# Kernel tuning notes

Measured on AMD Instinct MI355X. Metric: run time of the kernel, lower is better.

Reference implementation:

```python
import jax, jax.numpy as jnp
import numpy as np

EMBED_DIM = 1024
PROJ_DIM = 512
NUM_HEADS = 8
HEAD_DIM = PROJ_DIM // NUM_HEADS
B, L = 2, 2048


def setup_inputs() -> dict:
    key = jax.random.key(0)
    ks = jax.random.split(key, 7)
    s = lambda d: 1.0 / np.sqrt(d)
    return {
        "x": jax.random.normal(ks[0], (B, L, EMBED_DIM), jnp.float32),
        "proj_W": jax.random.normal(ks[1], (EMBED_DIM, PROJ_DIM), jnp.float32) * s(EMBED_DIM),
        "proj_b": jax.random.normal(ks[2], (PROJ_DIM,), jnp.float32) * 0.01,
        "attn_Wq": jax.random.normal(ks[3], (PROJ_DIM, NUM_HEADS, HEAD_DIM), jnp.float32) * s(PROJ_DIM),
        "attn_Wk": jax.random.normal(ks[4], (PROJ_DIM, NUM_HEADS, HEAD_DIM), jnp.float32) * s(PROJ_DIM),
        "attn_Wv": jax.random.normal(ks[5], (PROJ_DIM, NUM_HEADS, HEAD_DIM), jnp.float32) * s(PROJ_DIM),
        "out_W": jax.random.normal(ks[6], (NUM_HEADS * HEAD_DIM, EMBED_DIM), jnp.float32) * s(NUM_HEADS * HEAD_DIM),
    }


def reference(x, proj_W, proj_b, attn_Wq, attn_Wk, attn_Wv, out_W):
    # ReLU projection: (B, L, embed_dim) -> (B, L, proj_dim)
    p = jax.nn.relu(x @ proj_W + proj_b)
    # Per-head projections: (B, L, C) x (C, H, Dh) -> (B, H, L, Dh)
    q = jnp.einsum('blc,chd->bhld', p, attn_Wq)
    k = jnp.einsum('blc,chd->bhld', p, attn_Wk)
    v = jnp.einsum('blc,chd->bhld', p, attn_Wv)
    scale = 1.0 / np.sqrt(HEAD_DIM).astype(np.float32)
    scores = jnp.einsum('bhqd,bhkd->bhqk', q, k) * scale  # (B, H, L, L)
    weights = jax.nn.softmax(scores, axis=-1)
    heads = jnp.einsum('bhqk,bhkd->bhqd', weights, v)  # (B, H, L, Dh)
    heads = heads.transpose(0, 2, 1, 3).reshape(p.shape[0], p.shape[1], NUM_HEADS * HEAD_DIM)
    return heads @ out_W  # (B, L, embed_dim)
```

## Files before the change

### kernel.cpp

```cpp
#include <hip/hip_runtime.h>
#include <math.h>

#define BATCH 2
#define SEQ 2048
#define BL (BATCH * SEQ)
#define EMBED 1024
#define PROJ 512
#define NHEADS 8
#define HDIM 64
#define QKVN (3 * PROJ)

typedef _Float16 half8 __attribute__((ext_vector_type(8)));
typedef float floatx4 __attribute__((ext_vector_type(4)));

__global__ __launch_bounds__(256) void trconv(const float* __restrict__ src,
                                              _Float16* __restrict__ dst,
                                              int K, int N, float scale) {
    __shared__ float tile[64][65];
    const int t  = threadIdx.x;
    const int n0 = blockIdx.x * 64;
    const int k0 = blockIdx.y * 64;
    const int tx = t & 63;
    const int ty = t >> 6;
#pragma unroll
    for (int i = 0; i < 16; ++i) {
        int k = ty * 16 + i;
        tile[k][tx] = src[(size_t)(k0 + k) * N + n0 + tx];
    }
    __syncthreads();
#pragma unroll
    for (int i = 0; i < 16; ++i) {
        int n = ty * 16 + i;
        dst[(size_t)(n0 + n) * K + k0 + tx] = (_Float16)(tile[tx][n] * scale);
    }
}

__global__ __launch_bounds__(256) void trans_v(const _Float16* __restrict__ v,
                                               _Float16* __restrict__ vt) {
    __shared__ _Float16 tile[64][72];
    const int t  = threadIdx.x;
    const int t0 = blockIdx.x * 64;
    const int h  = blockIdx.y;
    const int b  = blockIdx.z;
    {
        const int r = t >> 2, c0 = (t & 3) * 16;
        const _Float16* src = v + (size_t)(b * SEQ + t0 + r) * QKVN + h * HDIM + c0;
        *reinterpret_cast<half8*>(&tile[r][c0])     = *reinterpret_cast<const half8*>(src);
        *reinterpret_cast<half8*>(&tile[r][c0 + 8]) = *reinterpret_cast<const half8*>(src + 8);
    }
    __syncthreads();
    {
        const int c = t >> 2, k0 = (t & 3) * 16;
        half8 o1, o2;
#pragma unroll
        for (int i = 0; i < 8; ++i) { o1[i] = tile[k0 + i][c]; o2[i] = tile[k0 + 8 + i][c]; }
        _Float16* dst = vt + ((size_t)(b * NHEADS + h) * HDIM + c) * SEQ + t0 + k0;
        *reinterpret_cast<half8*>(dst)     = o1;
        *reinterpret_cast<half8*>(dst + 8) = o2;
    }
}

template <int A_F32, int BIASRELU, int C_F32>
__global__ __launch_bounds__(256) void gemm_mfma(const void* __restrict__ Ap,
                                                 const _Float16* __restrict__ Bt,
                                                 const float* __restrict__ bias,
                                                 void* __restrict__ Cp,
                                                 int M, int N, int K) {
    __shared__ _Float16 Ah[64][40];
    __shared__ _Float16 Bh[128][40];

    const int t  = threadIdx.x;
    const int w  = t >> 6;
    const int l  = t & 63;
    const int lr = l & 15;
    const int lg = l >> 4;
    const int bm = blockIdx.y * 64;
    const int bn = blockIdx.x * 128;
    const int wr = w >> 1;
    const int wc = w & 1;

    const int ar = t >> 2, ac = (t & 3) * 8;
    const int br = t >> 1, bc = (t & 1) * 16;

    floatx4 acc[2][4];
#pragma unroll
    for (int i = 0; i < 2; ++i)
#pragma unroll
        for (int j = 0; j < 4; ++j) acc[i][j] = (floatx4){0.f, 0.f, 0.f, 0.f};

    float4 af0, af1;
    half8 areg, breg0, breg1;

    const float* Af = (const float*)Ap;
    const _Float16* Ah16 = (const _Float16*)Ap;

    if (A_F32) {
        af0 = *reinterpret_cast<const float4*>(&Af[(size_t)(bm + ar) * K + ac]);
        af1 = *reinterpret_cast<const float4*>(&Af[(size_t)(bm + ar) * K + ac + 4]);
    } else {
        areg = *reinterpret_cast<const half8*>(&Ah16[(size_t)(bm + ar) * K + ac]);
    }
    breg0 = *reinterpret_cast<const half8*>(&Bt[(size_t)(bn + br) * K + bc]);
    breg1 = *reinterpret_cast<const half8*>(&Bt[(size_t)(bn + br) * K + bc + 8]);

    for (int kt = 0; kt < K; kt += 32) {
        if (A_F32) {
            half8 hcv;
            hcv[0] = (_Float16)af0.x; hcv[1] = (_Float16)af0.y;
            hcv[2] = (_Float16)af0.z; hcv[3] = (_Float16)af0.w;
            hcv[4] = (_Float16)af1.x; hcv[5] = (_Float16)af1.y;
            hcv[6] = (_Float16)af1.z; hcv[7] = (_Float16)af1.w;
            *reinterpret_cast<half8*>(&Ah[ar][ac]) = hcv;
        } else {
            *reinterpret_cast<half8*>(&Ah[ar][ac]) = areg;
        }
        *reinterpret_cast<half8*>(&Bh[br][bc])     = breg0;
        *reinterpret_cast<half8*>(&Bh[br][bc + 8]) = breg1;
        __syncthreads();

        if (kt + 32 < K) {
            if (A_F32) {
                af0 = *reinterpret_cast<const float4*>(&Af[(size_t)(bm + ar) * K + kt + 32 + ac]);
                af1 = *reinterpret_cast<const float4*>(&Af[(size_t)(bm + ar) * K + kt + 32 + ac + 4]);
            } else {
                areg = *reinterpret_cast<const half8*>(&Ah16[(size_t)(bm + ar) * K + kt + 32 + ac]);
            }
            breg0 = *reinterpret_cast<const half8*>(&Bt[(size_t)(bn + br) * K + kt + 32 + bc]);
            breg1 = *reinterpret_cast<const half8*>(&Bt[(size_t)(bn + br) * K + kt + 32 + bc + 8]);
        }

        half8 afr[2], bfr[4];
#pragma unroll
        for (int mf = 0; mf < 2; ++mf)
            afr[mf] = *reinterpret_cast<const half8*>(&Ah[wr * 32 + mf * 16 + lr][lg * 8]);
#pragma unroll
        for (int nf = 0; nf < 4; ++nf)
            bfr[nf] = *reinterpret_cast<const half8*>(&Bh[wc * 64 + nf * 16 + lr][lg * 8]);
#pragma unroll
        for (int mf = 0; mf < 2; ++mf)
#pragma unroll
            for (int nf = 0; nf < 4; ++nf)
                acc[mf][nf] = __builtin_amdgcn_mfma_f32_16x16x32_f16(afr[mf], bfr[nf], acc[mf][nf], 0, 0, 0);

        __syncthreads();
    }

#pragma unroll
    for (int mf = 0; mf < 2; ++mf)
#pragma unroll
        for (int nf = 0; nf < 4; ++nf) {
            const int n = bn + wc * 64 + nf * 16 + lr;
            float bs = 0.f;
            if (BIASRELU) bs = bias[n];
#pragma unroll
            for (int r = 0; r < 4; ++r) {
                const int m = bm + wr * 32 + mf * 16 + lg * 4 + r;
                float v = acc[mf][nf][r];
                if (BIASRELU) v = fmaxf(v + bs, 0.f);
                if (C_F32)
                    ((float*)Cp)[(size_t)m * N + n] = v;
                else
                    ((_Float16*)Cp)[(size_t)m * N + n] = (_Float16)v;
            }
        }
}

__global__ __launch_bounds__(256) void attn_mfma(const _Float16* __restrict__ Q,
                                                 const _Float16* __restrict__ K,
                                                 const _Float16* __restrict__ Vt,
                                                 _Float16* __restrict__ O) {
    __shared__ _Float16 Ks[64][72];
    __shared__ _Float16 Vs[64][72];
    __shared__ _Float16 Ps[4][16][72];

    const int t  = threadIdx.x;
    const int w  = t >> 6;
    const int l  = t & 63;
    const int lr = l & 15;
    const int lg = l >> 4;

    const int q0 = blockIdx.x * 64;
    const int h  = blockIdx.y;
    const int b  = blockIdx.z;
    const size_t base  = (size_t)b * SEQ * QKVN + (size_t)h * HDIM;
    const size_t vbase = (size_t)(b * NHEADS + h) * HDIM * SEQ;
    const size_t baseO = (size_t)b * SEQ * PROJ + (size_t)h * HDIM;

    half8 qf[2];
#pragma unroll
    for (int s = 0; s < 2; ++s) {
        const int qrow = q0 + w * 16 + lr;
        qf[s] = *reinterpret_cast<const half8*>(
            &Q[base + (size_t)qrow * QKVN + s * 32 + lg * 8]);
    }

    floatx4 o_acc[4];
#pragma unroll
    for (int j = 0; j < 4; ++j) o_acc[j] = (floatx4){0.f, 0.f, 0.f, 0.f};

    float m_s = -1e30f;
    float l_s = 0.f;

    const int rkv = t >> 2;
    const int d0  = (t & 3) * 16;

    half8 ka0, ka1, va0, va1;
    {
        const _Float16* kp = K + base + (size_t)rkv * QKVN + d0;
        ka0 = *reinterpret_cast<const half8*>(kp);
        ka1 = *reinterpret_cast<const half8*>(kp + 8);
        const _Float16* vp = Vt + vbase + (size_t)rkv * SEQ + d0;
        va0 = *reinterpret_cast<const half8*>(vp);
        va1 = *reinterpret_cast<const half8*>(vp + 8);
    }

    for (int kt = 0; kt < SEQ; kt += 64) {
        *reinterpret_cast<half8*>(&Ks[rkv][d0])     = ka0;
        *reinterpret_cast<half8*>(&Ks[rkv][d0 + 8]) = ka1;
        *reinterpret_cast<half8*>(&Vs[rkv][d0])     = va0;
        *reinterpret_cast<half8*>(&Vs[rkv][d0 + 8]) = va1;
        __syncthreads();

        if (kt + 64 < SEQ) {
            const _Float16* kp = K + base + (size_t)(kt + 64 + rkv) * QKVN + d0;
            ka0 = *reinterpret_cast<const half8*>(kp);
            ka1 = *reinterpret_cast<const half8*>(kp + 8);
            const _Float16* vp = Vt + vbase + (size_t)rkv * SEQ + kt + 64 + d0;
            va0 = *reinterpret_cast<const half8*>(vp);
            va1 = *reinterpret_cast<const half8*>(vp + 8);
        }

        floatx4 stv[4];
#pragma unroll
        for (int i = 0; i < 4; ++i) stv[i] = (floatx4){0.f, 0.f, 0.f, 0.f};
#pragma unroll
        for (int s = 0; s < 2; ++s)
#pragma unroll
            for (int mf = 0; mf < 4; ++mf) {
                half8 kfr = *reinterpret_cast<const half8*>(&Ks[mf * 16 + lr][s * 32 + lg * 8]);
                stv[mf] = __builtin_amdgcn_mfma_f32_16x16x32_f16(kfr, qf[s], stv[mf], 0, 0, 0);
            }

        float tm = -1e30f;
#pragma unroll
        for (int mf = 0; mf < 4; ++mf)
#pragma unroll
            for (int r = 0; r < 4; ++r) tm = fmaxf(tm, stv[mf][r]);
        tm = fmaxf(tm, __shfl_xor(tm, 16));
        tm = fmaxf(tm, __shfl_xor(tm, 32));
        float mn = fmaxf(m_s, tm);
        float fscale = __expf(m_s - mn);
        m_s = mn;
        float sum = 0.f;
#pragma unroll
        for (int mf = 0; mf < 4; ++mf)
#pragma unroll
            for (int r = 0; r < 4; ++r) {
                float p = __expf(stv[mf][r] - mn);
                stv[mf][r] = p;
                sum += p;
            }
        sum += __shfl_xor(sum, 16);
        sum += __shfl_xor(sum, 32);
        l_s = l_s * fscale + sum;

#pragma unroll
        for (int mf = 0; mf < 4; ++mf)
#pragma unroll
            for (int rp = 0; rp < 2; ++rp) {
                union { _Float16 hh[2]; unsigned int u; } pk;
                pk.hh[0] = (_Float16)stv[mf][2 * rp];
                pk.hh[1] = (_Float16)stv[mf][2 * rp + 1];
                *reinterpret_cast<unsigned int*>(
                    &Ps[w][lr][mf * 16 + lg * 4 + rp * 2]) = pk.u;
            }

#pragma unroll
        for (int r = 0; r < 4; ++r) {
            float f = __shfl(fscale, lg * 4 + r);
#pragma unroll
            for (int nf = 0; nf < 4; ++nf) o_acc[nf][r] *= f;
        }

#pragma unroll
        for (int s = 0; s < 2; ++s) {
            half8 pa = *reinterpret_cast<const half8*>(&Ps[w][lr][s * 32 + lg * 8]);
#pragma unroll
            for (int nf = 0; nf < 4; ++nf) {
                half8 vb = *reinterpret_cast<const half8*>(&Vs[nf * 16 + lr][s * 32 + lg * 8]);
                o_acc[nf] = __builtin_amdgcn_mfma_f32_16x16x32_f16(pa, vb, o_acc[nf], 0, 0, 0);
            }
        }

        __syncthreads();
    }

#pragma unroll
    for (int r = 0; r < 4; ++r) {
        float inv = 1.0f / __shfl(l_s, lg * 4 + r);
        const int qrow = q0 + w * 16 + lg * 4 + r;
#pragma unroll
        for (int nf = 0; nf < 4; ++nf)
            O[baseO + (size_t)qrow * PROJ + nf * 16 + lr] =
                (_Float16)(o_acc[nf][r] * inv);
    }
}

extern "C" void kernel_launch(void* const* d_in, const int* in_sizes, int n_in,
                              void* d_out, int out_size, void* d_ws, size_t ws_size,
                              hipStream_t stream) {
    const float* x  = (const float*)d_in[0];
    const float* pW = (const float*)d_in[1];
    const float* pb = (const float*)d_in[2];
    const float* Wq = (const float*)d_in[3];
    const float* Wk = (const float*)d_in[4];
    const float* Wv = (const float*)d_in[5];
    const float* oW = (const float*)d_in[6];
    float* out = (float*)d_out;

    _Float16* ws    = (_Float16*)d_ws;
    _Float16* p_h   = ws;
    _Float16* qkv   = p_h + (size_t)BL * PROJ;
    _Float16* hd    = qkv + (size_t)BL * QKVN;
    _Float16* pWt   = hd + (size_t)BL * PROJ;
    _Float16* qkvWt = pWt + (size_t)PROJ * EMBED;
    _Float16* oWt   = qkvWt + (size_t)QKVN * PROJ;
    _Float16* vtb   = oWt + (size_t)EMBED * PROJ;

    dim3 blk(256);

    trconv<<<dim3(PROJ / 64, EMBED / 64), blk, 0, stream>>>(pW, pWt, EMBED, PROJ, 1.0f);
    trconv<<<dim3(PROJ / 64, PROJ / 64), blk, 0, stream>>>(Wq, qkvWt, PROJ, PROJ, 0.125f);
    trconv<<<dim3(PROJ / 64, PROJ / 64), blk, 0, stream>>>(Wk, qkvWt + (size_t)PROJ * PROJ, PROJ, PROJ, 1.0f);
    trconv<<<dim3(PROJ / 64, PROJ / 64), blk, 0, stream>>>(Wv, qkvWt + (size_t)2 * PROJ * PROJ, PROJ, PROJ, 1.0f);
    trconv<<<dim3(EMBED / 64, PROJ / 64), blk, 0, stream>>>(oW, oWt, PROJ, EMBED, 1.0f);

    gemm_mfma<1, 1, 0><<<dim3(PROJ / 128, BL / 64), blk, 0, stream>>>(
        (const void*)x, pWt, pb, (void*)p_h, BL, PROJ, EMBED);

    gemm_mfma<0, 0, 0><<<dim3(QKVN / 128, BL / 64), blk, 0, stream>>>(
        (const void*)p_h, qkvWt, nullptr, (void*)qkv, BL, QKVN, PROJ);

    trans_v<<<dim3(SEQ / 64, NHEADS, BATCH), blk, 0, stream>>>(qkv + 2 * PROJ, vtb);

    attn_mfma<<<dim3(SEQ / 64, NHEADS, BATCH), blk, 0, stream>>>(
        qkv, qkv + PROJ, vtb, hd);

    gemm_mfma<0, 0, 1><<<dim3(EMBED / 128, BL / 64), blk, 0, stream>>>(
        (const void*)hd, oWt, nullptr, (void*)out, BL, EMBED, PROJ);
}
```

Before: 121.8 us.

## Split attention over KV halves with merge kernel, shrink GEMM tiles, use exp2

Attention now splits the key/value sequence into two halves per query tile, doubling the block count. Each half writes unnormalized fp32 partial outputs plus running max and sum, and a new merge kernel combines them into the fp16 head output. The GEMM tile width drops from 128 to 64 to launch more blocks on the many-CU GPU. Softmax switches to exp2 with log2(e) folded into the Q weight scale. This trades extra fp32 partial-output traffic, an extra launch and smaller GEMM tiles with less reuse for better occupancy.

```diff
diff --git a/kernel.cpp b/kernel.cpp
--- a/kernel.cpp
+++ b/kernel.cpp
@@ -9,6 +9,8 @@
 #define NHEADS 8
 #define HDIM 64
 #define QKVN (3 * PROJ)
+#define KVSPLIT 2
+#define KVHALF (SEQ / KVSPLIT)
 
 typedef _Float16 half8 __attribute__((ext_vector_type(8)));
 typedef float floatx4 __attribute__((ext_vector_type(4)));
@@ -67,7 +69,7 @@
                                                  void* __restrict__ Cp,
                                                  int M, int N, int K) {
     __shared__ _Float16 Ah[64][40];
-    __shared__ _Float16 Bh[128][40];
+    __shared__ _Float16 Bh[64][40];
 
     const int t  = threadIdx.x;
     const int w  = t >> 6;
@@ -75,21 +77,20 @@
     const int lr = l & 15;
     const int lg = l >> 4;
     const int bm = blockIdx.y * 64;
-    const int bn = blockIdx.x * 128;
+    const int bn = blockIdx.x * 64;
     const int wr = w >> 1;
     const int wc = w & 1;
 
     const int ar = t >> 2, ac = (t & 3) * 8;
-    const int br = t >> 1, bc = (t & 1) * 16;
-
-    floatx4 acc[2][4];
+
+    floatx4 acc[2][2];
 #pragma unroll
     for (int i = 0; i < 2; ++i)
 #pragma unroll
-        for (int j = 0; j < 4; ++j) acc[i][j] = (floatx4){0.f, 0.f, 0.f, 0.f};
+        for (int j = 0; j < 2; ++j) acc[i][j] = (floatx4){0.f, 0.f, 0.f, 0.f};
 
     float4 af0, af1;
-    half8 areg, breg0, breg1;
+    half8 areg, breg;
 
     const float* Af = (const float*)Ap;
     const _Float16* Ah16 = (const _Float16*)Ap;
@@ -100,8 +101,7 @@
     } else {
         areg = *reinterpret_cast<const half8*>(&Ah16[(size_t)(bm + ar) * K + ac]);
     }
-    breg0 = *reinterpret_cast<const half8*>(&Bt[(size_t)(bn + br) * K + bc]);
-    breg1 = *reinterpret_cast<const half8*>(&Bt[(size_t)(bn + br) * K + bc + 8]);
+    breg = *reinterpret_cast<const half8*>(&Bt[(size_t)(bn + ar) * K + ac]);
 
     for (int kt = 0; kt < K; kt += 32) {
         if (A_F32) {
@@ -114,8 +114,7 @@
         } else {
             *reinterpret_cast<half8*>(&Ah[ar][ac]) = areg;
         }
-        *reinterpret_cast<half8*>(&Bh[br][bc])     = breg0;
-        *reinterpret_cast<half8*>(&Bh[br][bc + 8]) = breg1;
+        *reinterpret_cast<half8*>(&Bh[ar][ac]) = breg;
         __syncthreads();
 
         if (kt + 32 < K) {
@@ -125,21 +124,20 @@
             } else {
                 areg = *reinterpret_cast<const half8*>(&Ah16[(size_t)(bm + ar) * K + kt + 32 + ac]);
             }
-            breg0 = *reinterpret_cast<const half8*>(&Bt[(size_t)(bn + br) * K + kt + 32 + bc]);
-            breg1 = *reinterpret_cast<const half8*>(&Bt[(size_t)(bn + br) * K + kt + 32 + bc + 8]);
-        }
-
-        half8 afr[2], bfr[4];
+            breg = *reinterpret_cast<const half8*>(&Bt[(size_t)(bn + ar) * K + kt + 32 + ac]);
+        }
+
+        half8 afr[2], bfr[2];
 #pragma unroll
         for (int mf = 0; mf < 2; ++mf)
             afr[mf] = *reinterpret_cast<const half8*>(&Ah[wr * 32 + mf * 16 + lr][lg * 8]);
 #pragma unroll
-        for (int nf = 0; nf < 4; ++nf)
-            bfr[nf] = *reinterpret_cast<const half8*>(&Bh[wc * 64 + nf * 16 + lr][lg * 8]);
+        for (int nf = 0; nf < 2; ++nf)
+            bfr[nf] = *reinterpret_cast<const half8*>(&Bh[wc * 32 + nf * 16 + lr][lg * 8]);
 #pragma unroll
         for (int mf = 0; mf < 2; ++mf)
 #pragma unroll
-            for (int nf = 0; nf < 4; ++nf)
+            for (int nf = 0; nf < 2; ++nf)
                 acc[mf][nf] = __builtin_amdgcn_mfma_f32_16x16x32_f16(afr[mf], bfr[nf], acc[mf][nf], 0, 0, 0);
 
         __syncthreads();
@@ -148,8 +146,8 @@
 #pragma unroll
     for (int mf = 0; mf < 2; ++mf)
 #pragma unroll
-        for (int nf = 0; nf < 4; ++nf) {
-            const int n = bn + wc * 64 + nf * 16 + lr;
+        for (int nf = 0; nf < 2; ++nf) {
+            const int n = bn + wc * 32 + nf * 16 + lr;
             float bs = 0.f;
             if (BIASRELU) bs = bias[n];
 #pragma unroll
@@ -165,10 +163,11 @@
         }
 }
 
-__global__ __launch_bounds__(256) void attn_mfma(const _Float16* __restrict__ Q,
+__global__ __launch_bounds__(256) void attn_part(const _Float16* __restrict__ Q,
                                                  const _Float16* __restrict__ K,
                                                  const _Float16* __restrict__ Vt,
-                                                 _Float16* __restrict__ O) {
+                                                 float* __restrict__ Op,
+                                                 float* __restrict__ ml) {
     __shared__ _Float16 Ks[64][72];
     __shared__ _Float16 Vs[64][72];
     __shared__ _Float16 Ps[4][16][72];
@@ -179,12 +178,17 @@
     const int lr = l & 15;
     const int lg = l >> 4;
 
-    const int q0 = blockIdx.x * 64;
-    const int h  = blockIdx.y;
-    const int b  = blockIdx.z;
+    const int qt  = blockIdx.x >> 1;
+    const int kvh = blockIdx.x & 1;
+    const int q0  = qt * 64;
+    const int h   = blockIdx.y;
+    const int b   = blockIdx.z;
     const size_t base  = (size_t)b * SEQ * QKVN + (size_t)h * HDIM;
     const size_t vbase = (size_t)(b * NHEADS + h) * HDIM * SEQ;
-    const size_t baseO = (size_t)b * SEQ * PROJ + (size_t)h * HDIM;
+    const size_t poff  = (((size_t)kvh * BATCH + b) * NHEADS + h) * SEQ;
+
+    const int kt0  = kvh * KVHALF;
+    const int kend = kt0 + KVHALF;
 
     half8 qf[2];
 #pragma unroll
@@ -206,22 +210,22 @@
 
     half8 ka0, ka1, va0, va1;
     {
-        const _Float16* kp = K + base + (size_t)rkv * QKVN + d0;
+        const _Float16* kp = K + base + (size_t)(kt0 + rkv) * QKVN + d0;
         ka0 = *reinterpret_cast<const half8*>(kp);
         ka1 = *reinterpret_cast<const half8*>(kp + 8);
-        const _Float16* vp = Vt + vbase + (size_t)rkv * SEQ + d0;
+        const _Float16* vp = Vt + vbase + (size_t)rkv * SEQ + kt0 + d0;
         va0 = *reinterpret_cast<const half8*>(vp);
         va1 = *reinterpret_cast<const half8*>(vp + 8);
     }
 
-    for (int kt = 0; kt < SEQ; kt += 64) {
+    for (int kt = kt0; kt < kend; kt += 64) {
         *reinterpret_cast<half8*>(&Ks[rkv][d0])     = ka0;
         *reinterpret_cast<half8*>(&Ks[rkv][d0 + 8]) = ka1;
         *reinterpret_cast<half8*>(&Vs[rkv][d0])     = va0;
         *reinterpret_cast<half8*>(&Vs[rkv][d0 + 8]) = va1;
         __syncthreads();
 
-        if (kt + 64 < SEQ) {
+        if (kt + 64 < kend) {
             const _Float16* kp = K + base + (size_t)(kt + 64 + rkv) * QKVN + d0;
             ka0 = *reinterpret_cast<const half8*>(kp);
             ka1 = *reinterpret_cast<const half8*>(kp + 8);
@@ -249,14 +253,14 @@
         tm = fmaxf(tm, __shfl_xor(tm, 16));
         tm = fmaxf(tm, __shfl_xor(tm, 32));
         float mn = fmaxf(m_s, tm);
-        float fscale = __expf(m_s - mn);
+        float fscale = exp2f(m_s - mn);
         m_s = mn;
         float sum = 0.f;
 #pragma unroll
         for (int mf = 0; mf < 4; ++mf)
 #pragma unroll
             for (int r = 0; r < 4; ++r) {
-                float p = __expf(stv[mf][r] - mn);
+                float p = exp2f(stv[mf][r] - mn);
                 stv[mf][r] = p;
                 sum += p;
             }
@@ -297,13 +301,52 @@
 
 #pragma unroll
     for (int r = 0; r < 4; ++r) {
-        float inv = 1.0f / __shfl(l_s, lg * 4 + r);
         const int qrow = q0 + w * 16 + lg * 4 + r;
 #pragma unroll
         for (int nf = 0; nf < 4; ++nf)
-            O[baseO + (size_t)qrow * PROJ + nf * 16 + lr] =
-                (_Float16)(o_acc[nf][r] * inv);
-    }
+            Op[(poff + qrow) * HDIM + nf * 16 + lr] = o_acc[nf][r];
+    }
+    if (lg == 0) {
+        const int qrow = q0 + w * 16 + lr;
+        reinterpret_cast<float2*>(ml)[poff + qrow] = make_float2(m_s, l_s);
+    }
+}
+
+__global__ __launch_bounds__(256) void attn_merge(const float* __restrict__ Op,
+                                                  const float* __restrict__ ml,
+                                                  _Float16* __restrict__ hd) {
+    const int t  = threadIdx.x;
+    const int q  = blockIdx.x * 64 + (t >> 2);
+    const int d0 = (t & 3) * 16;
+    const int h  = blockIdx.y;
+    const int b  = blockIdx.z;
+
+    const size_t off0 = ((size_t)b * NHEADS + h) * SEQ + q;
+    const size_t off1 = ((size_t)(BATCH + b) * NHEADS + h) * SEQ + q;
+
+    float2 ml0 = reinterpret_cast<const float2*>(ml)[off0];
+    float2 ml1 = reinterpret_cast<const float2*>(ml)[off1];
+    float m  = fmaxf(ml0.x, ml1.x);
+    float a0 = exp2f(ml0.x - m);
+    float a1 = exp2f(ml1.x - m);
+    float inv = 1.0f / (ml0.y * a0 + ml1.y * a1);
+    a0 *= inv; a1 *= inv;
+
+    const float* p0 = Op + off0 * HDIM + d0;
+    const float* p1 = Op + off1 * HDIM + d0;
+    half8 o[2];
+#pragma unroll
+    for (int i = 0; i < 4; ++i) {
+        float4 v0 = reinterpret_cast<const float4*>(p0)[i];
+        float4 v1 = reinterpret_cast<const float4*>(p1)[i];
+        o[i >> 1][(i & 1) * 4 + 0] = (_Float16)(v0.x * a0 + v1.x * a1);
+        o[i >> 1][(i & 1) * 4 + 1] = (_Float16)(v0.y * a0 + v1.y * a1);
+        o[i >> 1][(i & 1) * 4 + 2] = (_Float16)(v0.z * a0 + v1.z * a1);
+        o[i >> 1][(i & 1) * 4 + 3] = (_Float16)(v0.w * a0 + v1.w * a1);
+    }
+    _Float16* dst = hd + (size_t)(b * SEQ + q) * PROJ + h * HDIM + d0;
+    *reinterpret_cast<half8*>(dst)     = o[0];
+    *reinterpret_cast<half8*>(dst + 8) = o[1];
 }
 
 extern "C" void kernel_launch(void* const* d_in, const int* in_sizes, int n_in,
@@ -326,26 +369,29 @@
     _Float16* qkvWt = pWt + (size_t)PROJ * EMBED;
     _Float16* oWt   = qkvWt + (size_t)QKVN * PROJ;
     _Float16* vtb   = oWt + (size_t)EMBED * PROJ;
+    float*    Opart = (float*)(vtb + (size_t)BATCH * NHEADS * HDIM * SEQ);
+    float*    mlb   = Opart + (size_t)KVSPLIT * BATCH * NHEADS * SEQ * HDIM;
 
     dim3 blk(256);
 
     trconv<<<dim3(PROJ / 64, EMBED / 64), blk, 0, stream>>>(pW, pWt, EMBED, PROJ, 1.0f);
-    trconv<<<dim3(PROJ / 64, PROJ / 64), blk, 0, stream>>>(Wq, qkvWt, PROJ, PROJ, 0.125f);
+    trconv<<<dim3(PROJ / 64, PROJ / 64), blk, 0, stream>>>(Wq, qkvWt, PROJ, PROJ, 0.125f * 1.44269504f);
     trconv<<<dim3(PROJ / 64, PROJ / 64), blk, 0, stream>>>(Wk, qkvWt + (size_t)PROJ * PROJ, PROJ, PROJ, 1.0f);
     trconv<<<dim3(PROJ / 64, PROJ / 64), blk, 0, stream>>>(Wv, qkvWt + (size_t)2 * PROJ * PROJ, PROJ, PROJ, 1.0f);
     trconv<<<dim3(EMBED / 64, PROJ / 64), blk, 0, stream>>>(oW, oWt, PROJ, EMBED, 1.0f);
 
-    gemm_mfma<1, 1, 0><<<dim3(PROJ / 128, BL / 64), blk, 0, stream>>>(
+    gemm_mfma<1, 1, 0><<<dim3(PROJ / 64, BL / 64), blk, 0, stream>>>(
         (const void*)x, pWt, pb, (void*)p_h, BL, PROJ, EMBED);
 
-    gemm_mfma<0, 0, 0><<<dim3(QKVN / 128, BL / 64), blk, 0, stream>>>(
+    gemm_mfma<0, 0, 0><<<dim3(QKVN / 64, BL / 64), blk, 0, stream>>>(
         (const void*)p_h, qkvWt, nullptr, (void*)qkv, BL, QKVN, PROJ);
 
     trans_v<<<dim3(SEQ / 64, NHEADS, BATCH), blk, 0, stream>>>(qkv + 2 * PROJ, vtb);
 
-    attn_mfma<<<dim3(SEQ / 64, NHEADS, BATCH), blk, 0, stream>>>(
-        qkv, qkv + PROJ, vtb, hd);
-
-    gemm_mfma<0, 0, 1><<<dim3(EMBED / 128, BL / 64), blk, 0, stream>>>(
+    attn_part<<<dim3((SEQ / 64) * KVSPLIT, NHEADS, BATCH), blk, 0, stream>>>(
+        qkv, qkv + PROJ, vtb, Opart, mlb);
+    attn_merge<<<dim3(SEQ / 64, NHEADS, BATCH), blk, 0, stream>>>(Opart, mlb, hd);
+
+    gemm_mfma<0, 0, 1><<<dim3(EMBED / 64, BL / 64), blk, 0, stream>>>(
         (const void*)hd, oWt, nullptr, (void*)out, BL, EMBED, PROJ);
 }
```

Result: no change. 122.9 us (+0.9%).
